# Optimization experiments

Measured on AMD Instinct MI355X. Metric: run time of the kernel, lower is better.

## Reference

```python
import jax, jax.numpy as jnp
import numpy as np
import math

PS = 8          # patch_size
OUT_C = 16      # out_channels
D_MODEL = 64
P_STATE = 32
BANDLIMIT = 1.0
STEP_SCALE = 1.0  # dt1 reference rate


def _ln(x, g, b, eps=1e-5):
    mu = jnp.mean(x, -1, keepdims=True)
    var = jnp.mean((x - mu) ** 2, -1, keepdims=True)
    return (x - mu) * jax.lax.rsqrt(var + eps) * g + b


def _forward(x, W_embed, b_embed, g1, beta1, Lambda_re, Lambda_im, B_re, B_im,
             C_re, C_im, D, log_step, g2, beta2, W_enc, W_dec, g3, beta3, W_out, b_out):
    b, t, h, w = x.shape
    hp, wp = h // PS, w // PS
    n = hp * wp
    # patchify: [b,t,h,w] -> [b,t,n,ps*ps]
    xp = x.reshape(b, t, hp, PS, wp, PS).transpose(0, 1, 2, 4, 3, 5).reshape(b, t, n, PS * PS)
    xe = xp @ W_embed.T + b_embed                              # [b,t,n,d]
    u = xe.transpose(0, 2, 1, 3).reshape(b * n, t, D_MODEL)    # [(b n), t, d]

    # ---- S5Block: pre-norm -> diagonal SSM -> gelu + residual -> GEGLU FFN ----
    fx = _ln(u, g1, beta1)
    Lam = Lambda_re + 1j * Lambda_im                           # [P] complex eigenvalues
    step = STEP_SCALE * jnp.exp(log_step)                      # [P]
    Lbar = jnp.exp(Lam * step)                                 # ZOH: A_bar
    Bbar = ((Lbar - 1.0) / Lam)[:, None] * (B_re + 1j * B_im)  # ZOH: B_bar [P,d]
    # bandlimit mask on C (freqs = step*|Im(Lambda)|/(2pi) < bandlimit/2)
    freqs = step * jnp.abs(Lambda_im) / (2.0 * math.pi)
    mask = (freqs < BANDLIMIT * 0.5).astype(C_re.dtype)
    Cc = (C_re + 1j * C_im) * mask[None, :]                    # [d,P]

    Bu = jnp.einsum('ntd,pd->ntp', fx.astype(jnp.complex64), Bbar)   # [(bn),t,P]
    A = jnp.broadcast_to(Lbar.astype(jnp.complex64), (1, t, P_STATE))

    def comb(e1, e2):
        a1, b1 = e1
        a2, b2 = e2
        return a1 * a2, a2 * b1 + b2

    _, xs = jax.lax.associative_scan(comb, (A, Bu), axis=1)    # x_k = A*x_{k-1} + Bu_k (x_0 = 0)
    ys = jnp.einsum('ntp,dp->ntd', xs, Cc).real + fx * D       # y = Re(C x) + D u
    xb = jax.nn.gelu(ys, approximate=False) + fx

    fx2 = _ln(xb, g2, beta2)
    enc = fx2 @ W_enc.T                                        # [(bn),t,2d]
    a, gate = jnp.split(enc, 2, axis=-1)
    xb = (a * jax.nn.gelu(gate, approximate=False)) @ W_dec.T + fx2

    # ---- take last timestep, project, unpatchify ----
    x_last = xb[:, -1, :]                                      # [(bn), d]
    proj = _ln(x_last, g3, beta3) @ W_out.T + b_out            # [(bn), C*ps*ps]
    y = proj.reshape(b, hp, wp, OUT_C, PS, PS).transpose(0, 3, 1, 4, 2, 5).reshape(b, OUT_C, h, w)
    return y


def setup_inputs() -> dict:
    key = jax.random.key(0)
    ks = jax.random.split(key, 12)
    d, P, pp = D_MODEL, P_STATE, PS * PS
    return dict(
        x=jax.random.normal(ks[0], (8, 15, 480, 640), jnp.float32),
        W_embed=jax.random.normal(ks[1], (d, pp), jnp.float32) / math.sqrt(pp),
        b_embed=jnp.zeros((d,), jnp.float32),
        g1=jnp.ones((d,), jnp.float32), beta1=jnp.zeros((d,), jnp.float32),
        Lambda_re=-0.5 * jnp.ones((P,), jnp.float32),
        Lambda_im=math.pi * (1.0 + jnp.arange(P, dtype=jnp.float32)),
        B_re=jax.random.normal(ks[2], (P, d), jnp.float32) / math.sqrt(d),
        B_im=jax.random.normal(ks[3], (P, d), jnp.float32) / math.sqrt(d),
        C_re=jax.random.normal(ks[4], (d, P), jnp.float32) / math.sqrt(P),
        C_im=jax.random.normal(ks[5], (d, P), jnp.float32) / math.sqrt(P),
        D=jax.random.normal(ks[6], (d,), jnp.float32),
        log_step=jax.random.uniform(ks[7], (P,), jnp.float32, math.log(1e-3), math.log(1e-1)),
        g2=jnp.ones((d,), jnp.float32), beta2=jnp.zeros((d,), jnp.float32),
        W_enc=jax.random.normal(ks[8], (2 * d, d), jnp.float32) / math.sqrt(d),
        W_dec=jax.random.normal(ks[9], (d, d), jnp.float32) / math.sqrt(d),
        g3=jnp.ones((d,), jnp.float32), beta3=jnp.zeros((d,), jnp.float32),
        W_out=jax.random.normal(ks[10], (OUT_C * pp, d), jnp.float32) / math.sqrt(d),
        b_out=jnp.zeros((OUT_C * pp,), jnp.float32),
    )


def reference(x, W_embed, b_embed, g1, beta1, Lambda_re, Lambda_im, B_re, B_im,
              C_re, C_im, D, log_step, g2, beta2, W_enc, W_dec, g3, beta3, W_out, b_out):
    return _forward(x, W_embed, b_embed, g1, beta1, Lambda_re, Lambda_im, B_re, B_im,
                    C_re, C_im, D, log_step, g2, beta2, W_enc, W_dec, g3, beta3, W_out, b_out)
```

## Files before the change

kernel.cpp:

```cpp
#include <hip/hip_runtime.h>
#include <math.h>


typedef __attribute__((ext_vector_type(8))) short short8;
typedef __attribute__((ext_vector_type(4))) short short4v;
typedef __attribute__((ext_vector_type(4))) float f32x4;

#define MFMA16(a, b, c) __builtin_amdgcn_mfma_f32_16x16x32_bf16((a), (b), (c), 0, 0, 0)

__device__ __forceinline__ short f2bf(float f) {
  union { float f; unsigned u; } v; v.f = f;
  unsigned r = (v.u + 0x7fffu + ((v.u >> 16) & 1u)) >> 16;
  return (short)r;
}
__device__ __forceinline__ float geluf(float x) {
  return 0.5f * x * (1.0f + erff(x * 0.70710678118654752f));
}
__device__ __forceinline__ float sum4(float4 v) { return v.x + v.y + v.z + v.w; }
__device__ __forceinline__ float dot4(float4 v) { return v.x*v.x + v.y*v.y + v.z*v.z + v.w*v.w; }

__device__ __forceinline__ void bbar_factors(const float* Lre, const float* Lim,
                                             const float* lstep, int p,
                                             float& fre, float& fim) {
  float st = expf(lstep[p]);
  float lr = Lre[p], li = Lim[p];
  float er = expf(lr * st);
  float lbr = er * cosf(li * st), lbi = er * sinf(li * st);
  float u = lbr - 1.0f, v = lbi;
  float den = lr * lr + li * li;
  fre = (u * lr + v * li) / den;
  fim = (v * lr - u * li) / den;
}

__global__ __launch_bounds__(256) void k0_prep(
    const float* __restrict__ W_embed, const float* __restrict__ g1,
    const float* __restrict__ be1, const float* __restrict__ Lre,
    const float* __restrict__ Lim, const float* __restrict__ Bre,
    const float* __restrict__ Bim, const float* __restrict__ Cre,
    const float* __restrict__ Cim, const float* __restrict__ lstep,
    const float* __restrict__ W_enc, const float* __restrict__ W_dec,
    const float* __restrict__ W_out, short* __restrict__ wimg,
    float* __restrict__ bu0) {
  const int bid = blockIdx.x;
  if (bid == 44) {
    int q = threadIdx.x;
    if (q < 64) {
      int c = q >> 5, p = q & 31;
      float fre, fim; bbar_factors(Lre, Lim, lstep, p, fre, fim);
      float s = 0.f;
      for (int d = 0; d < 64; ++d) {
        float br = Bre[p * 64 + d], bi = Bim[p * 64 + d];
        float val = c ? (fre * bi + fim * br) : (fre * br - fim * bi);
        s += be1[d] * val;
      }
      bu0[q] = s;
    }
    return;
  }
  const int w = threadIdx.x >> 6, lane = threadIdx.x & 63;
  const int l15 = lane & 15, qd = lane >> 4;
  const int f = bid * 4 + w;
  short v[8];
  if (f < 8) {
    int nt = f >> 1, kt = f & 1, n = nt * 16 + l15, k0 = kt * 32 + qd * 8;
#pragma unroll
    for (int j = 0; j < 8; ++j) v[j] = f2bf(W_embed[n * 64 + k0 + j]);
  } else if (f < 16) {
    int fi = f - 8, nt = fi >> 1, kt = fi & 1;
    int rq = nt * 16 + l15, c = rq >> 5, p = rq & 31, d0 = kt * 32 + qd * 8;
    float fre, fim; bbar_factors(Lre, Lim, lstep, p, fre, fim);
#pragma unroll
    for (int j = 0; j < 8; ++j) {
      int d = d0 + j;
      float br = Bre[p * 64 + d], bi = Bim[p * 64 + d];
      float val = c ? (fre * bi + fim * br) : (fre * br - fim * bi);
      v[j] = f2bf(g1[d] * val);
    }
  } else if (f < 24) {
    int fi = f - 16, nt = fi >> 1, kt = fi & 1;
    int d = nt * 16 + l15, q0 = kt * 32 + qd * 8;
#pragma unroll
    for (int j = 0; j < 8; ++j) {
      int qq = q0 + j, p = qq & 31;
      float stp = expf(lstep[p]);
      float fr = stp * fabsf(Lim[p]) * (1.0f / 6.28318530717958648f);
      float m = (fr < 0.5f) ? 1.f : 0.f;
      float val = (qq < 32) ? Cre[d * 32 + p] * m : -Cim[d * 32 + p] * m;
      v[j] = f2bf(val);
    }
  } else if (f < 40) {
    int fi = f - 24, nt = fi >> 1, kt = fi & 1, row = nt * 16 + l15;
#pragma unroll
    for (int j = 0; j < 8; ++j) v[j] = f2bf(W_enc[row * 64 + kt * 32 + qd * 8 + j]);
  } else if (f < 48) {
    int fi = f - 40, kt = fi & 1, row = (fi >> 1) * 16 + l15;
#pragma unroll
    for (int j = 0; j < 8; ++j) v[j] = f2bf(W_dec[row * 64 + kt * 32 + qd * 8 + j]);
  } else {
    int fi = f - 48, nt = fi >> 1, kt = fi & 1, row = nt * 16 + l15;
#pragma unroll
    for (int j = 0; j < 8; ++j) v[j] = f2bf(W_out[row * 64 + kt * 32 + qd * 8 + j]);
  }
  short8 sv;
#pragma unroll
  for (int j = 0; j < 8; ++j) sv[j] = v[j];
  *(short8*)&wimg[(f * 64 + lane) * 8] = sv;
}

__device__ __forceinline__ void ln_stats(const f32x4* tl, f32x4& mean, f32x4& rstd) {
  f32x4 s = tl[0] + tl[1] + tl[2] + tl[3];
  f32x4 s2 = tl[0] * tl[0] + tl[1] * tl[1] + tl[2] * tl[2] + tl[3] * tl[3];
#pragma unroll
  for (int m = 1; m < 16; m <<= 1) {
#pragma unroll
    for (int i = 0; i < 4; ++i) {
      s[i] += __shfl_xor(s[i], m);
      s2[i] += __shfl_xor(s2[i], m);
    }
  }
  mean = s * 0.015625f;
  f32x4 var = s2 * 0.015625f - mean * mean;
#pragma unroll
  for (int i = 0; i < 4; ++i) rstd[i] = rsqrtf(var[i] + 1e-5f);
}

__device__ __forceinline__ void stage_CtoA(short* st, const f32x4* tiles,
                                           int qd, int l15, short8* out) {
#pragma unroll
  for (int nt = 0; nt < 4; ++nt)
#pragma unroll
    for (int r = 0; r < 4; ++r)
      st[(qd * 4 + r) * 68 + nt * 16 + l15] = f2bf(tiles[nt][r]);
  __asm__ volatile("s_waitcnt lgkmcnt(0)" ::: "memory");
#pragma unroll
  for (int kt = 0; kt < 2; ++kt) {
    const short* sp = st + l15 * 68 + kt * 32 + qd * 8;
    short4v lo = *(const short4v*)sp;
    short4v hi = *(const short4v*)(sp + 4);
    short8 o;
    o[0] = lo[0]; o[1] = lo[1]; o[2] = lo[2]; o[3] = lo[3];
    o[4] = hi[0]; o[5] = hi[1]; o[6] = hi[2]; o[7] = hi[3];
    out[kt] = o;
  }
  __asm__ volatile("s_waitcnt lgkmcnt(0)" ::: "memory");
}

__global__ __launch_bounds__(128) void k1_fused(
    const float* __restrict__ x, const short* __restrict__ wimg_g,
    const float* __restrict__ bu0_g, const float* __restrict__ Lre,
    const float* __restrict__ Lim, const float* __restrict__ lstep,
    const float* __restrict__ g1, const float* __restrict__ be1,
    const float* __restrict__ bemb, const float* __restrict__ Dv,
    const float* __restrict__ g2, const float* __restrict__ be2,
    float* __restrict__ xlast) {
  __shared__ short wimg[48 * 512];
  __shared__ short stage[2][16 * 68];
  {
    float4* dst = (float4*)wimg;
    const float4* src = (const float4*)wimg_g;
    for (int i = threadIdx.x; i < 3072; i += 128) dst[i] = src[i];
  }
  __syncthreads();

  const int wv = threadIdx.x >> 6;
  const int lane = threadIdx.x & 63;
  const int l15 = lane & 15, qd = lane >> 4;
  short* st = &stage[wv][0];

  const int sbase = (blockIdx.x * 2 + wv) * 16;
  const int b_i = sbase / 4800;
  const int pr = sbase % 4800;
  const int ph = pr / 80;
  const int pw0 = pr % 80;

  const float* xbase = x + ((b_i * 15) * 480 + ph * 8) * 640 + (pw0 + l15) * 8;

  float g1c[4], b1c[4], bec[4], Dc[4], g2c[4], b2c[4], bu0c[4];
#pragma unroll
  for (int nt = 0; nt < 4; ++nt) {
    int col = nt * 16 + l15;
    g1c[nt] = g1[col]; b1c[nt] = be1[col]; bec[nt] = bemb[col];
    Dc[nt] = Dv[col];  g2c[nt] = g2[col];  b2c[nt] = be2[col];
    bu0c[nt] = bu0_g[col];
  }
  float st0 = expf(lstep[l15]), st1 = expf(lstep[l15 + 16]);
  float er0 = expf(Lre[l15] * st0), er1 = expf(Lre[l15 + 16] * st1);
  float lbr0 = er0 * cosf(Lim[l15] * st0), lbi0 = er0 * sinf(Lim[l15] * st0);
  float lbr1 = er1 * cosf(Lim[l15 + 16] * st1), lbi1 = er1 * sinf(Lim[l15 + 16] * st1);

  const f32x4 zf = {0.f, 0.f, 0.f, 0.f};
  f32x4 state[4] = {zf, zf, zf, zf};
  f32x4 xh[4];

  for (int t = 0; t < 15; ++t) {
    const float* xt = xbase + t * 307200;
    short8 pa[2];
#pragma unroll
    for (int kt = 0; kt < 2; ++kt) {
      const float* rp = xt + (kt * 4 + qd) * 640;
      float4 v0 = *(const float4*)rp;
      float4 v1 = *(const float4*)(rp + 4);
      short8 p8;
      p8[0] = f2bf(v0.x); p8[1] = f2bf(v0.y); p8[2] = f2bf(v0.z); p8[3] = f2bf(v0.w);
      p8[4] = f2bf(v1.x); p8[5] = f2bf(v1.y); p8[6] = f2bf(v1.z); p8[7] = f2bf(v1.w);
      pa[kt] = p8;
    }
    f32x4 c1[4];
#pragma unroll
    for (int nt = 0; nt < 4; ++nt) {
      f32x4 acc = zf;
      acc = MFMA16(pa[0], *(const short8*)&wimg[(nt * 2 + 0) * 512 + lane * 8], acc);
      acc = MFMA16(pa[1], *(const short8*)&wimg[(nt * 2 + 1) * 512 + lane * 8], acc);
      c1[nt] = acc + bec[nt];
    }
    f32x4 mean, rstd;
    ln_stats(c1, mean, rstd);
#pragma unroll
    for (int nt = 0; nt < 4; ++nt) xh[nt] = (c1[nt] - mean) * rstd;
    short8 xa[2];
    stage_CtoA(st, xh, qd, l15, xa);
    f32x4 t0 = state[0], t1 = state[1], t2 = state[2], t3 = state[3];
    state[0] = lbr0 * t0 - lbi0 * t2 + bu0c[0];
    state[1] = lbr1 * t1 - lbi1 * t3 + bu0c[1];
    state[2] = lbr0 * t2 + lbi0 * t0 + bu0c[2];
    state[3] = lbr1 * t3 + lbi1 * t1 + bu0c[3];
#pragma unroll
    for (int nt = 0; nt < 4; ++nt) {
      state[nt] = MFMA16(xa[0], *(const short8*)&wimg[(8 + nt * 2 + 0) * 512 + lane * 8], state[nt]);
      state[nt] = MFMA16(xa[1], *(const short8*)&wimg[(8 + nt * 2 + 1) * 512 + lane * 8], state[nt]);
    }
  }

  f32x4 fxl[4];
#pragma unroll
  for (int nt = 0; nt < 4; ++nt) fxl[nt] = xh[nt] * g1c[nt] + b1c[nt];

  short8 xsa[2];
  stage_CtoA(st, state, qd, l15, xsa);
  f32x4 ys[4];
#pragma unroll
  for (int nt = 0; nt < 4; ++nt) {
    f32x4 acc = fxl[nt] * Dc[nt];
    acc = MFMA16(xsa[0], *(const short8*)&wimg[(16 + nt * 2 + 0) * 512 + lane * 8], acc);
    acc = MFMA16(xsa[1], *(const short8*)&wimg[(16 + nt * 2 + 1) * 512 + lane * 8], acc);
    ys[nt] = acc;
  }
  f32x4 xbv[4];
#pragma unroll
  for (int nt = 0; nt < 4; ++nt)
#pragma unroll
    for (int i = 0; i < 4; ++i) xbv[nt][i] = geluf(ys[nt][i]) + fxl[nt][i];

  f32x4 mean2, rstd2;
  ln_stats(xbv, mean2, rstd2);
  f32x4 fx2[4];
#pragma unroll
  for (int nt = 0; nt < 4; ++nt)
    fx2[nt] = (xbv[nt] - mean2) * rstd2 * g2c[nt] + b2c[nt];

  short8 fa[2];
  stage_CtoA(st, fx2, qd, l15, fa);
  f32x4 e[8];
#pragma unroll
  for (int m = 0; m < 8; ++m) {
    f32x4 acc = zf;
    acc = MFMA16(fa[0], *(const short8*)&wimg[(24 + m * 2 + 0) * 512 + lane * 8], acc);
    acc = MFMA16(fa[1], *(const short8*)&wimg[(24 + m * 2 + 1) * 512 + lane * 8], acc);
    e[m] = acc;
  }
  f32x4 hv[4];
#pragma unroll
  for (int nt = 0; nt < 4; ++nt)
#pragma unroll
    for (int i = 0; i < 4; ++i) hv[nt][i] = e[nt][i] * geluf(e[nt + 4][i]);

  short8 ha[2];
  stage_CtoA(st, hv, qd, l15, ha);
#pragma unroll
  for (int nt = 0; nt < 4; ++nt) {
    f32x4 acc = fx2[nt];
    acc = MFMA16(ha[0], *(const short8*)&wimg[(40 + nt * 2 + 0) * 512 + lane * 8], acc);
    acc = MFMA16(ha[1], *(const short8*)&wimg[(40 + nt * 2 + 1) * 512 + lane * 8], acc);
#pragma unroll
    for (int r = 0; r < 4; ++r)
      xlast[(sbase + qd * 4 + r) * 64 + nt * 16 + l15] = acc[r];
  }
}

__global__ __launch_bounds__(256) void k2_head(
    const float* __restrict__ xlast, const short* __restrict__ wout_img,
    const float* __restrict__ g3, const float* __restrict__ be3,
    const float* __restrict__ b_out, float* __restrict__ y) {
  __shared__ short wo[32 * 512];
  const int nqb = blockIdx.x & 3;
  const int mblk = blockIdx.x >> 2;
  {
    float4* dst = (float4*)wo;
    const float4* src = (const float4*)(wout_img + nqb * 32 * 512);
    for (int i = threadIdx.x; i < 2048; i += 256) dst[i] = src[i];
  }
  __syncthreads();
  const int wv = threadIdx.x >> 6, lane = threadIdx.x & 63;
  const int l15 = lane & 15, qd = lane >> 4;
  const int sbase = mblk * 64 + wv * 16;
  const int nq0 = nqb * 256;
  const int seq = sbase + l15;
  const float* xr = xlast + seq * 64;
  float4 a0 = *(const float4*)(xr + qd * 8);
  float4 a1 = *(const float4*)(xr + qd * 8 + 4);
  float4 a2 = *(const float4*)(xr + 32 + qd * 8);
  float4 a3 = *(const float4*)(xr + 32 + qd * 8 + 4);
  float sum = sum4(a0) + sum4(a1) + sum4(a2) + sum4(a3);
  float ssq = dot4(a0) + dot4(a1) + dot4(a2) + dot4(a3);
  sum += __shfl_xor(sum, 16); sum += __shfl_xor(sum, 32);
  ssq += __shfl_xor(ssq, 16); ssq += __shfl_xor(ssq, 32);
  float mean = sum * (1.f / 64.f);
  float rstd = rsqrtf(ssq * (1.f / 64.f) - mean * mean + 1e-5f);
  float4 ga = *(const float4*)(g3 + qd * 8);
  float4 gb = *(const float4*)(g3 + qd * 8 + 4);
  float4 gc = *(const float4*)(g3 + 32 + qd * 8);
  float4 gd2 = *(const float4*)(g3 + 32 + qd * 8 + 4);
  float4 ba = *(const float4*)(be3 + qd * 8);
  float4 bb = *(const float4*)(be3 + qd * 8 + 4);
  float4 bc = *(const float4*)(be3 + 32 + qd * 8);
  float4 bd = *(const float4*)(be3 + 32 + qd * 8 + 4);
#define ZC(av, gv, bv) f2bf(((av)-mean) * rstd * (gv) + (bv))
  short8 za0, za1;
  za0[0] = ZC(a0.x, ga.x, ba.x); za0[1] = ZC(a0.y, ga.y, ba.y);
  za0[2] = ZC(a0.z, ga.z, ba.z); za0[3] = ZC(a0.w, ga.w, ba.w);
  za0[4] = ZC(a1.x, gb.x, bb.x); za0[5] = ZC(a1.y, gb.y, bb.y);
  za0[6] = ZC(a1.z, gb.z, bb.z); za0[7] = ZC(a1.w, gb.w, bb.w);
  za1[0] = ZC(a2.x, gc.x, bc.x); za1[1] = ZC(a2.y, gc.y, bc.y);
  za1[2] = ZC(a2.z, gc.z, bc.z); za1[3] = ZC(a2.w, gc.w, bc.w);
  za1[4] = ZC(a3.x, gd2.x, bd.x); za1[5] = ZC(a3.y, gd2.y, bd.y);
  za1[6] = ZC(a3.z, gd2.z, bd.z); za1[7] = ZC(a3.w, gd2.w, bd.w);
#undef ZC
  int ob[4];
#pragma unroll
  for (int r = 0; r < 4; ++r) {
    int sr = sbase + qd * 4 + r;
    int bi = sr / 4800, prr = sr % 4800;
    int phh = prr / 80, pww = prr % 80;
    ob[r] = (bi * 16 * 480 + phh * 8) * 640 + pww * 8;
  }
#pragma unroll
  for (int nt = 0; nt < 16; ++nt) {
    int o = nq0 + nt * 16 + l15;
    float bo = b_out[o];
    f32x4 acc = {bo, bo, bo, bo};
    acc = MFMA16(za0, *(const short8*)&wo[(nt * 2 + 0) * 512 + lane * 8], acc);
    acc = MFMA16(za1, *(const short8*)&wo[(nt * 2 + 1) * 512 + lane * 8], acc);
    int c = o >> 6, pi = (o >> 3) & 7, pj = o & 7;
    int off = c * 307200 + pi * 640 + pj;
#pragma unroll
    for (int r = 0; r < 4; ++r) y[ob[r] + off] = acc[r];
  }
}

extern "C" void kernel_launch(void* const* d_in, const int* in_sizes, int n_in,
                              void* d_out, int out_size, void* d_ws, size_t ws_size,
                              hipStream_t stream) {
  const float* x       = (const float*)d_in[0];
  const float* W_embed = (const float*)d_in[1];
  const float* b_embed = (const float*)d_in[2];
  const float* g1      = (const float*)d_in[3];
  const float* beta1   = (const float*)d_in[4];
  const float* Lre     = (const float*)d_in[5];
  const float* Lim     = (const float*)d_in[6];
  const float* Bre     = (const float*)d_in[7];
  const float* Bim     = (const float*)d_in[8];
  const float* Cre     = (const float*)d_in[9];
  const float* Cim     = (const float*)d_in[10];
  const float* Dv      = (const float*)d_in[11];
  const float* lstep   = (const float*)d_in[12];
  const float* g2      = (const float*)d_in[13];
  const float* beta2   = (const float*)d_in[14];
  const float* W_enc   = (const float*)d_in[15];
  const float* W_dec   = (const float*)d_in[16];
  const float* g3      = (const float*)d_in[17];
  const float* beta3   = (const float*)d_in[18];
  const float* W_out   = (const float*)d_in[19];
  const float* b_out   = (const float*)d_in[20];
  float* y = (float*)d_out;

  short* wimg = (short*)d_ws;
  float* bu0  = (float*)((char*)d_ws + 176 * 1024);
  float* xlast = (float*)((char*)d_ws + 180 * 1024);

  k0_prep<<<dim3(45), dim3(256), 0, stream>>>(W_embed, g1, beta1, Lre, Lim,
                                              Bre, Bim, Cre, Cim, lstep,
                                              W_enc, W_dec, W_out, wimg, bu0);
  k1_fused<<<dim3(1200), dim3(128), 0, stream>>>(x, wimg, bu0, Lre, Lim, lstep,
                                                 g1, beta1, b_embed, Dv, g2,
                                                 beta2, xlast);
  k2_head<<<dim3(2400), dim3(256), 0, stream>>>(xlast, wimg + 48 * 512, g3,
                                                beta3, b_out, y);
}
```

Measured before the change: 357.8 us.

## Swap MFMA operand roles to keep activations in registers, dropping LDS staging

Swaps the MFMA operand order so weights are the A operand and activations the B operand, and permutes the prepacked weight rows (ecmap) so each accumulator fragment feeds the next MFMA directly. This removes the per-step LDS round trip and waitcnt stalls that transposed C fragments into A fragments. The change also prefetches the next timestep's x into registers, moves to 256-thread blocks, writes the intermediate in a transposed layout, and lets the head kernel store y as float4. The risks are more register pressure and strided, less coalesced xlastT writes in k1 and reads in k2.

```diff
diff --git a/kernel.cpp b/kernel.cpp
--- a/kernel.cpp
+++ b/kernel.cpp
@@ -3,7 +3,6 @@
 
 
 typedef __attribute__((ext_vector_type(8))) short short8;
-typedef __attribute__((ext_vector_type(4))) short short4v;
 typedef __attribute__((ext_vector_type(4))) float f32x4;
 
 #define MFMA16(a, b, c) __builtin_amdgcn_mfma_f32_16x16x32_bf16((a), (b), (c), 0, 0, 0)
@@ -16,9 +15,15 @@
 __device__ __forceinline__ float geluf(float x) {
   return 0.5f * x * (1.0f + erff(x * 0.70710678118654752f));
 }
-__device__ __forceinline__ float sum4(float4 v) { return v.x + v.y + v.z + v.w; }
-__device__ __forceinline__ float dot4(float4 v) { return v.x*v.x + v.y*v.y + v.z*v.z + v.w*v.w; }
-
+__device__ __forceinline__ short8 packfrag(const f32x4& a, const f32x4& b) {
+  short8 o;
+  o[0] = f2bf(a[0]); o[1] = f2bf(a[1]); o[2] = f2bf(a[2]); o[3] = f2bf(a[3]);
+  o[4] = f2bf(b[0]); o[5] = f2bf(b[1]); o[6] = f2bf(b[2]); o[7] = f2bf(b[3]);
+  return o;
+}
+__device__ __forceinline__ int ecmap(int i, int m) {
+  return (i >> 1) * 32 + (m >> 2) * 8 + (i & 1) * 4 + (m & 3);
+}
 __device__ __forceinline__ void bbar_factors(const float* Lre, const float* Lim,
                                              const float* lstep, int p,
                                              float& fre, float& fim) {
@@ -58,46 +63,46 @@
     return;
   }
   const int w = threadIdx.x >> 6, lane = threadIdx.x & 63;
-  const int l15 = lane & 15, qd = lane >> 4;
+  const int m = lane & 15, qd = lane >> 4;
   const int f = bid * 4 + w;
   short v[8];
   if (f < 8) {
-    int nt = f >> 1, kt = f & 1, n = nt * 16 + l15, k0 = kt * 32 + qd * 8;
-#pragma unroll
-    for (int j = 0; j < 8; ++j) v[j] = f2bf(W_embed[n * 64 + k0 + j]);
+    int i = f >> 1, kt = f & 1, chan = ecmap(i, m), k0 = kt * 32 + qd * 8;
+#pragma unroll
+    for (int j = 0; j < 8; ++j) v[j] = f2bf(W_embed[chan * 64 + k0 + j]);
   } else if (f < 16) {
-    int fi = f - 8, nt = fi >> 1, kt = fi & 1;
-    int rq = nt * 16 + l15, c = rq >> 5, p = rq & 31, d0 = kt * 32 + qd * 8;
+    int fi = f - 8, i = fi >> 1, kt = fi & 1;
+    int comp = i & 1, p = (i >> 1) * 16 + m, d0 = kt * 32 + qd * 8;
     float fre, fim; bbar_factors(Lre, Lim, lstep, p, fre, fim);
 #pragma unroll
     for (int j = 0; j < 8; ++j) {
       int d = d0 + j;
       float br = Bre[p * 64 + d], bi = Bim[p * 64 + d];
-      float val = c ? (fre * bi + fim * br) : (fre * br - fim * bi);
+      float val = comp ? (fre * bi + fim * br) : (fre * br - fim * bi);
       v[j] = f2bf(g1[d] * val);
     }
   } else if (f < 24) {
-    int fi = f - 16, nt = fi >> 1, kt = fi & 1;
-    int d = nt * 16 + l15, q0 = kt * 32 + qd * 8;
+    int fi = f - 16, i = fi >> 1, kt = fi & 1, chan = ecmap(i, m);
 #pragma unroll
     for (int j = 0; j < 8; ++j) {
-      int qq = q0 + j, p = qq & 31;
+      int comp = j >> 2, p = kt * 16 + qd * 4 + (j & 3);
       float stp = expf(lstep[p]);
       float fr = stp * fabsf(Lim[p]) * (1.0f / 6.28318530717958648f);
-      float m = (fr < 0.5f) ? 1.f : 0.f;
-      float val = (qq < 32) ? Cre[d * 32 + p] * m : -Cim[d * 32 + p] * m;
+      float msk = (fr < 0.5f) ? 1.f : 0.f;
+      float val = comp ? -Cim[chan * 32 + p] * msk : Cre[chan * 32 + p] * msk;
       v[j] = f2bf(val);
     }
   } else if (f < 40) {
-    int fi = f - 24, nt = fi >> 1, kt = fi & 1, row = nt * 16 + l15;
+    int fi = f - 24, i = fi >> 1, kt = fi & 1;
+    int row = (i < 4) ? ecmap(i, m) : 64 + ecmap(i - 4, m);
 #pragma unroll
     for (int j = 0; j < 8; ++j) v[j] = f2bf(W_enc[row * 64 + kt * 32 + qd * 8 + j]);
   } else if (f < 48) {
-    int fi = f - 40, kt = fi & 1, row = (fi >> 1) * 16 + l15;
+    int fi = f - 40, i = fi >> 1, kt = fi & 1, row = ecmap(i, m);
 #pragma unroll
     for (int j = 0; j < 8; ++j) v[j] = f2bf(W_dec[row * 64 + kt * 32 + qd * 8 + j]);
   } else {
-    int fi = f - 48, nt = fi >> 1, kt = fi & 1, row = nt * 16 + l15;
+    int fi = f - 48, i = fi >> 1, kt = fi & 1, row = i * 16 + m;
 #pragma unroll
     for (int j = 0; j < 8; ++j) v[j] = f2bf(W_out[row * 64 + kt * 32 + qd * 8 + j]);
   }
@@ -107,166 +112,156 @@
   *(short8*)&wimg[(f * 64 + lane) * 8] = sv;
 }
 
-__device__ __forceinline__ void ln_stats(const f32x4* tl, f32x4& mean, f32x4& rstd) {
-  f32x4 s = tl[0] + tl[1] + tl[2] + tl[3];
-  f32x4 s2 = tl[0] * tl[0] + tl[1] * tl[1] + tl[2] * tl[2] + tl[3] * tl[3];
-#pragma unroll
-  for (int m = 1; m < 16; m <<= 1) {
-#pragma unroll
-    for (int i = 0; i < 4; ++i) {
-      s[i] += __shfl_xor(s[i], m);
-      s2[i] += __shfl_xor(s2[i], m);
-    }
-  }
-  mean = s * 0.015625f;
-  f32x4 var = s2 * 0.015625f - mean * mean;
-#pragma unroll
-  for (int i = 0; i < 4; ++i) rstd[i] = rsqrtf(var[i] + 1e-5f);
-}
-
-__device__ __forceinline__ void stage_CtoA(short* st, const f32x4* tiles,
-                                           int qd, int l15, short8* out) {
-#pragma unroll
-  for (int nt = 0; nt < 4; ++nt)
-#pragma unroll
-    for (int r = 0; r < 4; ++r)
-      st[(qd * 4 + r) * 68 + nt * 16 + l15] = f2bf(tiles[nt][r]);
-  __asm__ volatile("s_waitcnt lgkmcnt(0)" ::: "memory");
-#pragma unroll
-  for (int kt = 0; kt < 2; ++kt) {
-    const short* sp = st + l15 * 68 + kt * 32 + qd * 8;
-    short4v lo = *(const short4v*)sp;
-    short4v hi = *(const short4v*)(sp + 4);
-    short8 o;
-    o[0] = lo[0]; o[1] = lo[1]; o[2] = lo[2]; o[3] = lo[3];
-    o[4] = hi[0]; o[5] = hi[1]; o[6] = hi[2]; o[7] = hi[3];
-    out[kt] = o;
-  }
-  __asm__ volatile("s_waitcnt lgkmcnt(0)" ::: "memory");
-}
-
-__global__ __launch_bounds__(128) void k1_fused(
+__global__ __launch_bounds__(256) void k1_fused(
     const float* __restrict__ x, const short* __restrict__ wimg_g,
     const float* __restrict__ bu0_g, const float* __restrict__ Lre,
     const float* __restrict__ Lim, const float* __restrict__ lstep,
     const float* __restrict__ g1, const float* __restrict__ be1,
     const float* __restrict__ bemb, const float* __restrict__ Dv,
     const float* __restrict__ g2, const float* __restrict__ be2,
-    float* __restrict__ xlast) {
+    float* __restrict__ xlastT) {
   __shared__ short wimg[48 * 512];
-  __shared__ short stage[2][16 * 68];
   {
     float4* dst = (float4*)wimg;
     const float4* src = (const float4*)wimg_g;
-    for (int i = threadIdx.x; i < 3072; i += 128) dst[i] = src[i];
+    for (int i = threadIdx.x; i < 3072; i += 256) dst[i] = src[i];
   }
   __syncthreads();
-
-  const int wv = threadIdx.x >> 6;
-  const int lane = threadIdx.x & 63;
-  const int l15 = lane & 15, qd = lane >> 4;
-  short* st = &stage[wv][0];
-
-  const int sbase = (blockIdx.x * 2 + wv) * 16;
+#define WF(id) (*(const short8*)&wimg[(id) * 512 + lane * 8])
+
+  const int wv = threadIdx.x >> 6, lane = threadIdx.x & 63;
+  const int s = lane & 15, qd = lane >> 4;
+  const int sbase = (blockIdx.x * 4 + wv) * 16;
   const int b_i = sbase / 4800;
   const int pr = sbase % 4800;
   const int ph = pr / 80;
   const int pw0 = pr % 80;
-
-  const float* xbase = x + ((b_i * 15) * 480 + ph * 8) * 640 + (pw0 + l15) * 8;
-
-  float g1c[4], b1c[4], bec[4], Dc[4], g2c[4], b2c[4], bu0c[4];
+  const float* xbase = x + ((b_i * 15) * 480 + ph * 8) * 640 + (pw0 + s) * 8;
+
+  int cb[4];
+  f32x4 bec[4], bu0c[4];
 #pragma unroll
   for (int nt = 0; nt < 4; ++nt) {
-    int col = nt * 16 + l15;
-    g1c[nt] = g1[col]; b1c[nt] = be1[col]; bec[nt] = bemb[col];
-    Dc[nt] = Dv[col];  g2c[nt] = g2[col];  b2c[nt] = be2[col];
-    bu0c[nt] = bu0_g[col];
-  }
-  float st0 = expf(lstep[l15]), st1 = expf(lstep[l15 + 16]);
-  float er0 = expf(Lre[l15] * st0), er1 = expf(Lre[l15 + 16] * st1);
-  float lbr0 = er0 * cosf(Lim[l15] * st0), lbi0 = er0 * sinf(Lim[l15] * st0);
-  float lbr1 = er1 * cosf(Lim[l15 + 16] * st1), lbi1 = er1 * sinf(Lim[l15 + 16] * st1);
+    cb[nt] = (nt >> 1) * 32 + qd * 8 + (nt & 1) * 4;
+    bec[nt] = *(const f32x4*)(bemb + cb[nt]);
+    bu0c[nt] = *(const f32x4*)(bu0_g + (nt & 1) * 32 + (nt >> 1) * 16 + qd * 4);
+  }
+  f32x4 lbr[2], lbi[2];
+#pragma unroll
+  for (int k = 0; k < 2; ++k)
+#pragma unroll
+    for (int r = 0; r < 4; ++r) {
+      int p = k * 16 + qd * 4 + r;
+      float st = expf(lstep[p]);
+      float er = expf(Lre[p] * st);
+      lbr[k][r] = er * cosf(Lim[p] * st);
+      lbi[k][r] = er * sinf(Lim[p] * st);
+    }
 
   const f32x4 zf = {0.f, 0.f, 0.f, 0.f};
   f32x4 state[4] = {zf, zf, zf, zf};
   f32x4 xh[4];
 
+  f32x4 vcur[4], vnext[4];
+#pragma unroll
+  for (int kt = 0; kt < 2; ++kt) {
+    const float* rp = xbase + (kt * 4 + qd) * 640;
+    vcur[kt * 2] = *(const f32x4*)rp;
+    vcur[kt * 2 + 1] = *(const f32x4*)(rp + 4);
+  }
+
   for (int t = 0; t < 15; ++t) {
-    const float* xt = xbase + t * 307200;
-    short8 pa[2];
-#pragma unroll
-    for (int kt = 0; kt < 2; ++kt) {
-      const float* rp = xt + (kt * 4 + qd) * 640;
-      float4 v0 = *(const float4*)rp;
-      float4 v1 = *(const float4*)(rp + 4);
-      short8 p8;
-      p8[0] = f2bf(v0.x); p8[1] = f2bf(v0.y); p8[2] = f2bf(v0.z); p8[3] = f2bf(v0.w);
-      p8[4] = f2bf(v1.x); p8[5] = f2bf(v1.y); p8[6] = f2bf(v1.z); p8[7] = f2bf(v1.w);
-      pa[kt] = p8;
-    }
+    if (t < 14) {
+      const float* xn = xbase + (t + 1) * 307200;
+#pragma unroll
+      for (int kt = 0; kt < 2; ++kt) {
+        const float* rp = xn + (kt * 4 + qd) * 640;
+        vnext[kt * 2] = *(const f32x4*)rp;
+        vnext[kt * 2 + 1] = *(const f32x4*)(rp + 4);
+      }
+    }
+    short8 pa0 = packfrag(vcur[0], vcur[1]);
+    short8 pa1 = packfrag(vcur[2], vcur[3]);
     f32x4 c1[4];
 #pragma unroll
-    for (int nt = 0; nt < 4; ++nt) {
-      f32x4 acc = zf;
-      acc = MFMA16(pa[0], *(const short8*)&wimg[(nt * 2 + 0) * 512 + lane * 8], acc);
-      acc = MFMA16(pa[1], *(const short8*)&wimg[(nt * 2 + 1) * 512 + lane * 8], acc);
-      c1[nt] = acc + bec[nt];
-    }
-    f32x4 mean, rstd;
-    ln_stats(c1, mean, rstd);
+    for (int i = 0; i < 4; ++i) {
+      f32x4 acc = MFMA16(WF(i * 2), pa0, zf);
+      acc = MFMA16(WF(i * 2 + 1), pa1, acc);
+      c1[i] = acc + bec[i];
+    }
+    float sm = 0.f, sq = 0.f;
+#pragma unroll
+    for (int nt = 0; nt < 4; ++nt)
+#pragma unroll
+      for (int i = 0; i < 4; ++i) { sm += c1[nt][i]; sq += c1[nt][i] * c1[nt][i]; }
+    sm += __shfl_xor(sm, 16); sq += __shfl_xor(sq, 16);
+    sm += __shfl_xor(sm, 32); sq += __shfl_xor(sq, 32);
+    float mean = sm * 0.015625f;
+    float rstd = rsqrtf(sq * 0.015625f - mean * mean + 1e-5f);
 #pragma unroll
     for (int nt = 0; nt < 4; ++nt) xh[nt] = (c1[nt] - mean) * rstd;
-    short8 xa[2];
-    stage_CtoA(st, xh, qd, l15, xa);
-    f32x4 t0 = state[0], t1 = state[1], t2 = state[2], t3 = state[3];
-    state[0] = lbr0 * t0 - lbi0 * t2 + bu0c[0];
-    state[1] = lbr1 * t1 - lbi1 * t3 + bu0c[1];
-    state[2] = lbr0 * t2 + lbi0 * t0 + bu0c[2];
-    state[3] = lbr1 * t3 + lbi1 * t1 + bu0c[3];
-#pragma unroll
-    for (int nt = 0; nt < 4; ++nt) {
-      state[nt] = MFMA16(xa[0], *(const short8*)&wimg[(8 + nt * 2 + 0) * 512 + lane * 8], state[nt]);
-      state[nt] = MFMA16(xa[1], *(const short8*)&wimg[(8 + nt * 2 + 1) * 512 + lane * 8], state[nt]);
-    }
-  }
-
+    short8 xa0 = packfrag(xh[0], xh[1]);
+    short8 xa1 = packfrag(xh[2], xh[3]);
+#pragma unroll
+    for (int k = 0; k < 2; ++k) {
+      f32x4 re = state[2 * k], im = state[2 * k + 1];
+      state[2 * k]     = lbr[k] * re - lbi[k] * im + bu0c[2 * k];
+      state[2 * k + 1] = lbr[k] * im + lbi[k] * re + bu0c[2 * k + 1];
+    }
+#pragma unroll
+    for (int i = 0; i < 4; ++i) {
+      state[i] = MFMA16(WF(8 + i * 2), xa0, state[i]);
+      state[i] = MFMA16(WF(8 + i * 2 + 1), xa1, state[i]);
+    }
+#pragma unroll
+    for (int q = 0; q < 4; ++q) vcur[q] = vnext[q];
+  }
+
+  f32x4 g1c[4], b1c[4], Dc[4], g2c[4], b2c[4];
+#pragma unroll
+  for (int nt = 0; nt < 4; ++nt) {
+    g1c[nt] = *(const f32x4*)(g1 + cb[nt]);
+    b1c[nt] = *(const f32x4*)(be1 + cb[nt]);
+    Dc[nt] = *(const f32x4*)(Dv + cb[nt]);
+    g2c[nt] = *(const f32x4*)(g2 + cb[nt]);
+    b2c[nt] = *(const f32x4*)(be2 + cb[nt]);
+  }
   f32x4 fxl[4];
 #pragma unroll
   for (int nt = 0; nt < 4; ++nt) fxl[nt] = xh[nt] * g1c[nt] + b1c[nt];
 
-  short8 xsa[2];
-  stage_CtoA(st, state, qd, l15, xsa);
-  f32x4 ys[4];
-#pragma unroll
-  for (int nt = 0; nt < 4; ++nt) {
-    f32x4 acc = fxl[nt] * Dc[nt];
-    acc = MFMA16(xsa[0], *(const short8*)&wimg[(16 + nt * 2 + 0) * 512 + lane * 8], acc);
-    acc = MFMA16(xsa[1], *(const short8*)&wimg[(16 + nt * 2 + 1) * 512 + lane * 8], acc);
-    ys[nt] = acc;
-  }
+  short8 xsa0 = packfrag(state[0], state[1]);
+  short8 xsa1 = packfrag(state[2], state[3]);
   f32x4 xbv[4];
 #pragma unroll
+  for (int i = 0; i < 4; ++i) {
+    f32x4 acc = fxl[i] * Dc[i];
+    acc = MFMA16(WF(16 + i * 2), xsa0, acc);
+    acc = MFMA16(WF(16 + i * 2 + 1), xsa1, acc);
+#pragma unroll
+    for (int r = 0; r < 4; ++r) xbv[i][r] = geluf(acc[r]) + fxl[i][r];
+  }
+  float sm2 = 0.f, sq2 = 0.f;
+#pragma unroll
   for (int nt = 0; nt < 4; ++nt)
 #pragma unroll
-    for (int i = 0; i < 4; ++i) xbv[nt][i] = geluf(ys[nt][i]) + fxl[nt][i];
-
-  f32x4 mean2, rstd2;
-  ln_stats(xbv, mean2, rstd2);
+    for (int i = 0; i < 4; ++i) { sm2 += xbv[nt][i]; sq2 += xbv[nt][i] * xbv[nt][i]; }
+  sm2 += __shfl_xor(sm2, 16); sq2 += __shfl_xor(sq2, 16);
+  sm2 += __shfl_xor(sm2, 32); sq2 += __shfl_xor(sq2, 32);
+  float mean2 = sm2 * 0.015625f;
+  float rstd2 = rsqrtf(sq2 * 0.015625f - mean2 * mean2 + 1e-5f);
   f32x4 fx2[4];
 #pragma unroll
   for (int nt = 0; nt < 4; ++nt)
     fx2[nt] = (xbv[nt] - mean2) * rstd2 * g2c[nt] + b2c[nt];
 
-  short8 fa[2];
-  stage_CtoA(st, fx2, qd, l15, fa);
+  short8 fa0 = packfrag(fx2[0], fx2[1]);
+  short8 fa1 = packfrag(fx2[2], fx2[3]);
   f32x4 e[8];
 #pragma unroll
-  for (int m = 0; m < 8; ++m) {
-    f32x4 acc = zf;
-    acc = MFMA16(fa[0], *(const short8*)&wimg[(24 + m * 2 + 0) * 512 + lane * 8], acc);
-    acc = MFMA16(fa[1], *(const short8*)&wimg[(24 + m * 2 + 1) * 512 + lane * 8], acc);
-    e[m] = acc;
+  for (int i = 0; i < 8; ++i) {
+    f32x4 acc = MFMA16(WF(24 + i * 2), fa0, zf);
+    e[i] = MFMA16(WF(24 + i * 2 + 1), fa1, acc);
   }
   f32x4 hv[4];
 #pragma unroll
@@ -274,21 +269,25 @@
 #pragma unroll
     for (int i = 0; i < 4; ++i) hv[nt][i] = e[nt][i] * geluf(e[nt + 4][i]);
 
-  short8 ha[2];
-  stage_CtoA(st, hv, qd, l15, ha);
-#pragma unroll
-  for (int nt = 0; nt < 4; ++nt) {
-    f32x4 acc = fx2[nt];
-    acc = MFMA16(ha[0], *(const short8*)&wimg[(40 + nt * 2 + 0) * 512 + lane * 8], acc);
-    acc = MFMA16(ha[1], *(const short8*)&wimg[(40 + nt * 2 + 1) * 512 + lane * 8], acc);
-#pragma unroll
-    for (int r = 0; r < 4; ++r)
-      xlast[(sbase + qd * 4 + r) * 64 + nt * 16 + l15] = acc[r];
-  }
+  short8 ha0 = packfrag(hv[0], hv[1]);
+  short8 ha1 = packfrag(hv[2], hv[3]);
+  f32x4 xo[4];
+#pragma unroll
+  for (int i = 0; i < 4; ++i) {
+    f32x4 acc = fx2[i];
+    acc = MFMA16(WF(40 + i * 2), ha0, acc);
+    xo[i] = MFMA16(WF(40 + i * 2 + 1), ha1, acc);
+  }
+#pragma unroll
+  for (int kt = 0; kt < 2; ++kt)
+#pragma unroll
+    for (int j = 0; j < 8; ++j)
+      xlastT[(kt * 32 + qd * 8 + j) * 38400 + sbase + s] = xo[2 * kt + (j >> 2)][j & 3];
+#undef WF
 }
 
 __global__ __launch_bounds__(256) void k2_head(
-    const float* __restrict__ xlast, const short* __restrict__ wout_img,
+    const float* __restrict__ xlastT, const short* __restrict__ wout_img,
     const float* __restrict__ g3, const float* __restrict__ be3,
     const float* __restrict__ b_out, float* __restrict__ y) {
   __shared__ short wo[32 * 512];
@@ -301,59 +300,52 @@
   }
   __syncthreads();
   const int wv = threadIdx.x >> 6, lane = threadIdx.x & 63;
-  const int l15 = lane & 15, qd = lane >> 4;
+  const int s = lane & 15, qd = lane >> 4;
   const int sbase = mblk * 64 + wv * 16;
+  const int seq = sbase + s;
   const int nq0 = nqb * 256;
-  const int seq = sbase + l15;
-  const float* xr = xlast + seq * 64;
-  float4 a0 = *(const float4*)(xr + qd * 8);
-  float4 a1 = *(const float4*)(xr + qd * 8 + 4);
-  float4 a2 = *(const float4*)(xr + 32 + qd * 8);
-  float4 a3 = *(const float4*)(xr + 32 + qd * 8 + 4);
-  float sum = sum4(a0) + sum4(a1) + sum4(a2) + sum4(a3);
-  float ssq = dot4(a0) + dot4(a1) + dot4(a2) + dot4(a3);
-  sum += __shfl_xor(sum, 16); sum += __shfl_xor(sum, 32);
-  ssq += __shfl_xor(ssq, 16); ssq += __shfl_xor(ssq, 32);
-  float mean = sum * (1.f / 64.f);
-  float rstd = rsqrtf(ssq * (1.f / 64.f) - mean * mean + 1e-5f);
-  float4 ga = *(const float4*)(g3 + qd * 8);
-  float4 gb = *(const float4*)(g3 + qd * 8 + 4);
-  float4 gc = *(const float4*)(g3 + 32 + qd * 8);
-  float4 gd2 = *(const float4*)(g3 + 32 + qd * 8 + 4);
-  float4 ba = *(const float4*)(be3 + qd * 8);
-  float4 bb = *(const float4*)(be3 + qd * 8 + 4);
-  float4 bc = *(const float4*)(be3 + 32 + qd * 8);
-  float4 bd = *(const float4*)(be3 + 32 + qd * 8 + 4);
-#define ZC(av, gv, bv) f2bf(((av)-mean) * rstd * (gv) + (bv))
-  short8 za0, za1;
-  za0[0] = ZC(a0.x, ga.x, ba.x); za0[1] = ZC(a0.y, ga.y, ba.y);
-  za0[2] = ZC(a0.z, ga.z, ba.z); za0[3] = ZC(a0.w, ga.w, ba.w);
-  za0[4] = ZC(a1.x, gb.x, bb.x); za0[5] = ZC(a1.y, gb.y, bb.y);
-  za0[6] = ZC(a1.z, gb.z, bb.z); za0[7] = ZC(a1.w, gb.w, bb.w);
-  za1[0] = ZC(a2.x, gc.x, bc.x); za1[1] = ZC(a2.y, gc.y, bc.y);
-  za1[2] = ZC(a2.z, gc.z, bc.z); za1[3] = ZC(a2.w, gc.w, bc.w);
-  za1[4] = ZC(a3.x, gd2.x, bd.x); za1[5] = ZC(a3.y, gd2.y, bd.y);
-  za1[6] = ZC(a3.z, gd2.z, bd.z); za1[7] = ZC(a3.w, gd2.w, bd.w);
-#undef ZC
-  int ob[4];
-#pragma unroll
-  for (int r = 0; r < 4; ++r) {
-    int sr = sbase + qd * 4 + r;
-    int bi = sr / 4800, prr = sr % 4800;
-    int phh = prr / 80, pww = prr % 80;
-    ob[r] = (bi * 16 * 480 + phh * 8) * 640 + pww * 8;
-  }
+
+  float vals[2][8];
+#pragma unroll
+  for (int kt = 0; kt < 2; ++kt)
+#pragma unroll
+    for (int j = 0; j < 8; ++j)
+      vals[kt][j] = xlastT[(kt * 32 + qd * 8 + j) * 38400 + seq];
+  float sm = 0.f, sq = 0.f;
+#pragma unroll
+  for (int kt = 0; kt < 2; ++kt)
+#pragma unroll
+    for (int j = 0; j < 8; ++j) { sm += vals[kt][j]; sq += vals[kt][j] * vals[kt][j]; }
+  sm += __shfl_xor(sm, 16); sq += __shfl_xor(sq, 16);
+  sm += __shfl_xor(sm, 32); sq += __shfl_xor(sq, 32);
+  float mean = sm * 0.015625f;
+  float rstd = rsqrtf(sq * 0.015625f - mean * mean + 1e-5f);
+
+  short8 zb[2];
+#pragma unroll
+  for (int kt = 0; kt < 2; ++kt) {
+    f32x4 ga = *(const f32x4*)(g3 + kt * 32 + qd * 8);
+    f32x4 gb = *(const f32x4*)(g3 + kt * 32 + qd * 8 + 4);
+    f32x4 ba = *(const f32x4*)(be3 + kt * 32 + qd * 8);
+    f32x4 bb = *(const f32x4*)(be3 + kt * 32 + qd * 8 + 4);
+#pragma unroll
+    for (int j = 0; j < 4; ++j) {
+      zb[kt][j] = f2bf((vals[kt][j] - mean) * rstd * ga[j] + ba[j]);
+      zb[kt][j + 4] = f2bf((vals[kt][j + 4] - mean) * rstd * gb[j] + bb[j]);
+    }
+  }
+  const int bi2 = seq / 4800, prr = seq % 4800;
+  const int phh = prr / 80, pww = prr % 80;
+  const int obase = (bi2 * 16 * 480 + phh * 8) * 640 + pww * 8;
+
 #pragma unroll
   for (int nt = 0; nt < 16; ++nt) {
-    int o = nq0 + nt * 16 + l15;
-    float bo = b_out[o];
-    f32x4 acc = {bo, bo, bo, bo};
-    acc = MFMA16(za0, *(const short8*)&wo[(nt * 2 + 0) * 512 + lane * 8], acc);
-    acc = MFMA16(za1, *(const short8*)&wo[(nt * 2 + 1) * 512 + lane * 8], acc);
-    int c = o >> 6, pi = (o >> 3) & 7, pj = o & 7;
-    int off = c * 307200 + pi * 640 + pj;
-#pragma unroll
-    for (int r = 0; r < 4; ++r) y[ob[r] + off] = acc[r];
+    int o0 = nq0 + nt * 16 + qd * 4;
+    f32x4 acc = *(const f32x4*)(b_out + o0);
+    acc = MFMA16(*(const short8*)&wo[(nt * 2 + 0) * 512 + lane * 8], zb[0], acc);
+    acc = MFMA16(*(const short8*)&wo[(nt * 2 + 1) * 512 + lane * 8], zb[1], acc);
+    int c = o0 >> 6, pi = (o0 >> 3) & 7, pj = o0 & 7;
+    *(f32x4*)&y[obase + c * 307200 + pi * 640 + pj] = acc;
   }
 }
 
@@ -384,15 +376,15 @@
   float* y = (float*)d_out;
 
   short* wimg = (short*)d_ws;
-  float* bu0  = (float*)((char*)d_ws + 176 * 1024);
-  float* xlast = (float*)((char*)d_ws + 180 * 1024);
+  float* bu0 = (float*)((char*)d_ws + 176 * 1024);
+  float* xlastT = (float*)((char*)d_ws + 180 * 1024);
 
   k0_prep<<<dim3(45), dim3(256), 0, stream>>>(W_embed, g1, beta1, Lre, Lim,
                                               Bre, Bim, Cre, Cim, lstep,
                                               W_enc, W_dec, W_out, wimg, bu0);
-  k1_fused<<<dim3(1200), dim3(128), 0, stream>>>(x, wimg, bu0, Lre, Lim, lstep,
-                                                 g1, beta1, b_embed, Dv, g2,
-                                                 beta2, xlast);
-  k2_head<<<dim3(2400), dim3(256), 0, stream>>>(xlast, wimg + 48 * 512, g3,
+  k1_fused<<<dim3(600), dim3(256), 0, stream>>>(x, wimg, bu0, Lre, Lim, lstep,
+                                                g1, beta1, b_embed, Dv, g2,
+                                                beta2, xlastT);
+  k2_head<<<dim3(2400), dim3(256), 0, stream>>>(xlastT, wimg + 48 * 512, g3,
                                                 beta3, b_out, y);
 }
```

Result: no change. 352.2 us (-1.6%).
